# Kernel tuning notes

Hardware: AMD Instinct MI355X
Metric: run time of the kernel (lower is better)

## Reference

```python
import jax, jax.numpy as jnp
import numpy as np

B, C, D, H, W_, CT = 2, 64, 12, 20, 40, 32


def setup_inputs() -> dict:
    key = jax.random.key(0)
    ks = jax.random.split(key, 8)
    def w(k, o, i):
        return jax.random.normal(k, (o, i), jnp.float32) / np.float32(np.sqrt(i))
    return dict(
        x=jax.random.normal(ks[0], (B, C, D, H, W_), jnp.float32),
        preds=jax.random.normal(ks[1], (B, D, H, W_), jnp.float32),
        Wq1=w(ks[2], CT, C), Wq2=w(ks[3], CT, CT),
        Wk1=w(ks[4], CT, C), Wk2=w(ks[5], CT, CT),
        Wv=w(ks[6], CT, C), Wo=w(ks[7], C, CT),
    )


def conv_bn_relu(x, Wm, eps=1e-5):
    # 1x1x1 Conv3d (no bias) + BatchNorm3d (batch stats, no affine) + ReLU
    y = jnp.einsum('bcdhw,oc->bodhw', x, Wm)
    mu = y.mean(axis=(0, 2, 3, 4), keepdims=True)
    var = y.var(axis=(0, 2, 3, 4), keepdims=True)
    return jax.nn.relu((y - mu) * jax.lax.rsqrt(var + eps))


def semantic_gather(x, preds):
    # Vectorized equivalent of the nested batch/disp-class loops:
    # per-pixel argmax over disparity planes, softmax within each argmax group,
    # scatter weighted feature into a dense (b, hw, d, c) tensor (zeros elsewhere).
    b, c, d, h, w = x.shape
    p = jax.nn.softmax(preds, axis=1).reshape(b, d, h * w).transpose(0, 2, 1)  # (b,hw,d)
    f = x.reshape(b, c, d, h * w).transpose(0, 3, 2, 1)                        # (b,hw,d,c)
    a = jnp.argmax(p, axis=-1)                                                 # (b,hw) segment ids
    pv = jnp.take_along_axis(p, a[..., None], axis=-1)[..., 0]                 # (b,hw) gathered prob

    def seg_softmax(vals, segs):
        # softmax over pixels sharing the same argmax disparity class
        m = jax.lax.stop_gradient(jax.ops.segment_max(vals, segs, num_segments=d))
        e = jnp.exp(vals - m[segs])
        s = jax.ops.segment_sum(e, segs, num_segments=d)
        return e / s[segs]

    wt = jax.vmap(seg_softmax)(pv, a)                                          # (b,hw)
    fg = jnp.take_along_axis(f, a[:, :, None, None], axis=2)[:, :, 0, :]       # (b,hw,c)
    oh = jax.nn.one_hot(a, d, dtype=x.dtype)                                   # (b,hw,d)
    feats_sl = oh[..., None] * (fg * wt[..., None])[:, :, None, :]             # (b,hw,d,c)
    return feats_sl.reshape(b, h, w, d, c).transpose(0, 4, 3, 1, 2)            # (b,c,d,h,w)


def reference(x, preds, Wq1, Wq2, Wk1, Wk2, Wv, Wo):
    feats_sl = semantic_gather(x, preds)
    key_feats = feats_sl + x
    # SelfAttentionBlock: query/key = 2 conv-bn-relu, value/out = 1 conv-bn-relu
    q = conv_bn_relu(conv_bn_relu(x, Wq1), Wq2)
    k = conv_bn_relu(conv_bn_relu(key_feats, Wk1), Wk2)
    v = conv_bn_relu(key_feats, Wv)
    b, ct, d, h, w = q.shape
    n = d * h * w
    qf = q.reshape(b, ct, n).transpose(0, 2, 1)   # (b,n,ct)
    kf = k.reshape(b, ct, n)                      # (b,ct,n)
    vf = v.reshape(b, ct, n).transpose(0, 2, 1)   # (b,n,ct)
    sim = jnp.einsum('bnc,bcm->bnm', qf, kf) * (ct ** -0.5)
    sim = jax.nn.softmax(sim, axis=-1)
    ctx = jnp.einsum('bnm,bmc->bnc', sim, vf).transpose(0, 2, 1).reshape(b, ct, d, h, w)
    return conv_bn_relu(ctx, Wo)
```

## Files before the change

### kernel.cpp

```cpp
#include <hip/hip_runtime.h>

#define NB 2
#define CIN 64
#define DD 12
#define HWP 800
#define NPOS 9600
#define CT 32
#define QKSCALE 0.25506601f
#define CSH 11.541560327f

typedef __attribute__((ext_vector_type(8))) short short8;
typedef __attribute__((ext_vector_type(16))) float f32x16;

__device__ __forceinline__ ushort f2bf(float x){
    union { float f; unsigned u; } v; v.f = x;
    unsigned r = v.u + 0x7fffu + ((v.u >> 16) & 1u);
    return (ushort)(r >> 16);
}

__global__ __launch_bounds__(256) void seg_kernel(const float* __restrict__ preds,
                                                  int* __restrict__ a, float* __restrict__ wt)
{
    int b = blockIdx.x / DD, seg = blockIdx.x % DD;
    __shared__ float lpv[HWP];
    __shared__ int   la[HWP];
    __shared__ float red[256];
    int t = threadIdx.x;
    for (int i=t; i<HWP; i+=256){
        const float* p = preds + (size_t)b*DD*HWP + i;
        float mx = -INFINITY; int am = 0;
        #pragma unroll
        for (int d=0; d<DD; ++d){ float v = p[d*HWP]; if (v > mx){ mx=v; am=d; } }
        float s = 0.f;
        #pragma unroll
        for (int d=0; d<DD; ++d) s += __expf(p[d*HWP]-mx);
        lpv[i] = 1.f/s; la[i] = am;
        if (seg == 0) a[b*HWP+i] = am;
    }
    __syncthreads();
    float mx = -INFINITY;
    for (int i=t; i<HWP; i+=256) if (la[i]==seg) mx = fmaxf(mx, lpv[i]);
    red[t]=mx; __syncthreads();
    for (int s=128; s>0; s>>=1){ if (t<s) red[t]=fmaxf(red[t],red[t+s]); __syncthreads(); }
    float m = red[0]; __syncthreads();
    if (m == -INFINITY) return;
    float sm = 0.f;
    for (int i=t; i<HWP; i+=256) if (la[i]==seg) sm += __expf(lpv[i]-m);
    red[t]=sm; __syncthreads();
    for (int s=128; s>0; s>>=1){ if (t<s) red[t]+=red[t+s]; __syncthreads(); }
    float ssum = red[0];
    for (int i=t; i<HWP; i+=256) if (la[i]==seg) wt[b*HWP+i] = __expf(lpv[i]-m)/ssum;
}

__global__ __launch_bounds__(256) void conv1_kernel(const float* __restrict__ x,
    const int* __restrict__ a, const float* __restrict__ wt,
    const float* __restrict__ Wq1, const float* __restrict__ Wk1, const float* __restrict__ Wv,
    float* __restrict__ q1, float* __restrict__ k1, float* __restrict__ v1,
    float* __restrict__ part)
{
    __shared__ float lw[6144];
    for (int i=threadIdx.x; i<2048; i+=256){ lw[i]=Wq1[i]; lw[2048+i]=Wk1[i]; lw[4096+i]=Wv[i]; }
    __syncthreads();
    int t = threadIdx.x;
    int posIdx = blockIdx.x*32 + (t&31);
    int g = t>>5;
    int b = posIdx / NPOS, pos = posIdx % NPOS;
    int d = pos / HWP, pix = pos % HWP;
    float fac = 1.f;
    if (a[b*HWP+pix] == d) fac += wt[b*HWP+pix];
    float acc[12];
    #pragma unroll
    for (int j=0;j<12;++j) acc[j]=0.f;
    const float* xb = x + (size_t)b*CIN*NPOS + pos;
    int chBase = g*12;
    for (int c=0;c<CIN;++c){
        float xv = xb[(size_t)c*NPOS];
        const float* wrow = &lw[chBase*64 + c];
        #pragma unroll
        for (int j=0;j<12;++j) acc[j] += xv * wrow[j*64];
    }
    #pragma unroll
    for (int j=0;j<12;++j){
        int ch = chBase + j;
        float val = acc[j];
        if (ch >= 32) val *= fac;
        acc[j] = val;
        if (ch < 32)       q1[((size_t)b*CT + ch)*NPOS + pos] = val;
        else if (ch < 64)  k1[((size_t)b*CT + (ch-32))*NPOS + pos] = val;
        else               v1[((size_t)b*CT + (ch-64))*NPOS + pos] = val;
    }
    #pragma unroll
    for (int j=0;j<12;++j){
        float s = acc[j], qs = acc[j]*acc[j];
        #pragma unroll
        for (int off=16; off; off>>=1){ s += __shfl_xor(s,off); qs += __shfl_xor(qs,off); }
        if ((t&31)==0){
            int ch = chBase+j;
            part[((size_t)ch*600 + blockIdx.x)*2]   = s;
            part[((size_t)ch*600 + blockIdx.x)*2+1] = qs;
        }
    }
}

__global__ __launch_bounds__(64) void statsfin_kernel(const float* __restrict__ part,
    float* __restrict__ mu, float* __restrict__ rs, int nblk)
{
    int ch = blockIdx.x;
    float s=0.f, q=0.f;
    for (int i=threadIdx.x; i<nblk; i+=64){
        s += part[((size_t)ch*nblk+i)*2];
        q += part[((size_t)ch*nblk+i)*2+1];
    }
    #pragma unroll
    for (int off=32; off; off>>=1){ s += __shfl_xor(s,off); q += __shfl_xor(q,off); }
    if (threadIdx.x==0){
        float m = s/19200.f;
        mu[ch]=m; rs[ch]=rsqrtf(q/19200.f - m*m + 1e-5f);
    }
}

__global__ __launch_bounds__(256) void conv2_kernel(const float* __restrict__ q1, const float* __restrict__ k1,
    const float* __restrict__ Wq2, const float* __restrict__ Wk2,
    const float* __restrict__ mu1, const float* __restrict__ rs1,
    float* __restrict__ q2, float* __restrict__ k2, float* __restrict__ part)
{
    __shared__ float lw[2048];
    for (int i=threadIdx.x; i<1024; i+=256){ lw[i]=Wq2[i]; lw[1024+i]=Wk2[i]; }
    __syncthreads();
    int t = threadIdx.x;
    int posIdx = blockIdx.x*32 + (t&31);
    int g = t>>5;
    int b = posIdx / NPOS, pos = posIdx % NPOS;
    const float* src = (g<4) ? q1 : k1;
    const float* wb  = (g<4) ? lw : (lw+1024);
    float* dst       = (g<4) ? q2 : k2;
    int so = (g<4) ? 0 : 32;
    int chBase = (g&3)*8;
    float acc[8];
    #pragma unroll
    for (int j=0;j<8;++j) acc[j]=0.f;
    for (int c=0;c<32;++c){
        float v = src[((size_t)b*CT + c)*NPOS + pos];
        float vn = fmaxf((v - mu1[so+c])*rs1[so+c], 0.f);
        const float* wrow = &wb[chBase*32 + c];
        #pragma unroll
        for (int j=0;j<8;++j) acc[j] += vn * wrow[j*32];
    }
    #pragma unroll
    for (int j=0;j<8;++j)
        dst[((size_t)b*CT + chBase + j)*NPOS + pos] = acc[j];
    #pragma unroll
    for (int j=0;j<8;++j){
        float s = acc[j], qs = acc[j]*acc[j];
        #pragma unroll
        for (int off=16; off; off>>=1){ s += __shfl_xor(s,off); qs += __shfl_xor(qs,off); }
        if ((t&31)==0){
            int ch = so + chBase + j;
            part[((size_t)ch*600 + blockIdx.x)*2]   = s;
            part[((size_t)ch*600 + blockIdx.x)*2+1] = qs;
        }
    }
}

__global__ __launch_bounds__(256) void pack_kernel(const float* __restrict__ q2, const float* __restrict__ k2,
    const float* __restrict__ v1,
    const float* __restrict__ mu2, const float* __restrict__ rs2,
    const float* __restrict__ muv, const float* __restrict__ rsv,
    ushort* __restrict__ Qbf, ushort* __restrict__ KP, ushort* __restrict__ VP)
{
    if (blockIdx.x < 75){
        int idx = blockIdx.x*256 + threadIdx.x;
        int b = idx / NPOS, pos = idx - b*NPOS;
        const float* qsrc = q2 + (size_t)b*CT*NPOS + pos;
        const float* ksrc = k2 + (size_t)b*CT*NPOS + pos;
        unsigned qw[16], kw[16];
        #pragma unroll
        for (int c2=0; c2<16; ++c2){
            int c0 = 2*c2, c1 = 2*c2+1;
            float a0 = fmaxf((qsrc[(size_t)c0*NPOS] - mu2[c0])*rs2[c0], 0.f)*QKSCALE;
            float a1 = fmaxf((qsrc[(size_t)c1*NPOS] - mu2[c1])*rs2[c1], 0.f)*QKSCALE;
            qw[c2] = (unsigned)f2bf(a0) | ((unsigned)f2bf(a1)<<16);
            float b0 = fmaxf((ksrc[(size_t)c0*NPOS] - mu2[32+c0])*rs2[32+c0], 0.f);
            float b1 = fmaxf((ksrc[(size_t)c1*NPOS] - mu2[32+c1])*rs2[32+c1], 0.f);
            kw[c2] = (unsigned)f2bf(b0) | ((unsigned)f2bf(b1)<<16);
        }
        uint4* qd = (uint4*)(Qbf + (size_t)idx*CT);
        #pragma unroll
        for (int j=0;j<4;++j)
            qd[j] = make_uint4(qw[4*j], qw[4*j+1], qw[4*j+2], qw[4*j+3]);
        int kb = pos >> 5, c = pos & 31;
        ushort* base = KP + ((size_t)(b*300 + kb))*1024;
        *(uint4*)(base + (c)*8)          = make_uint4(kw[0],kw[1],kw[2],kw[3]);
        *(uint4*)(base + (c+32)*8)       = make_uint4(kw[4],kw[5],kw[6],kw[7]);
        *(uint4*)(base + 512 + (c)*8)    = make_uint4(kw[8],kw[9],kw[10],kw[11]);
        *(uint4*)(base + 512 + (c+32)*8) = make_uint4(kw[12],kw[13],kw[14],kw[15]);
    } else {
        int idx = (blockIdx.x-75)*256 + threadIdx.x;
        int b = idx / 38400;
        int r = idx - b*38400;
        int c = r / 1200;
        int g8 = r - c*1200;
        int key = g8*8;
        int kb = g8 >> 2, q8 = g8 & 3;
        int p = q8 >> 1, hh = q8 & 1;
        const float* vs = v1 + ((size_t)b*CT + c)*NPOS + key;
        float m = muv[c], rr = rsv[c];
        unsigned wds[4];
        #pragma unroll
        for (int j=0;j<4;++j){
            float a0 = fmaxf((vs[2*j]   - m)*rr, 0.f);
            float a1 = fmaxf((vs[2*j+1] - m)*rr, 0.f);
            wds[j] = (unsigned)f2bf(a0) | ((unsigned)f2bf(a1)<<16);
        }
        *(uint4*)(VP + ((size_t)(b*300 + kb))*1024 + p*512 + (c + 32*hh)*8)
            = make_uint4(wds[0],wds[1],wds[2],wds[3]);
    }
}

__global__ __launch_bounds__(256) void attn_kernel(const ushort* __restrict__ Qbf,
    const ushort* __restrict__ KP, const ushort* __restrict__ VP,
    float* __restrict__ pacc, float* __restrict__ plsum)
{
    __shared__ float mrg[3][64][17];
    int xcd = blockIdx.x & 7, idx = blockIdx.x >> 3;
    int b = xcd >> 2;
    int qb = (xcd & 3)*75 + idx%75;
    int third = idx/75;
    int q0 = qb*32;
    int t = threadIdx.x, wv = t>>6, l = t&63;
    int c = l & 31, h = l >> 5;

    const char* QbU = (const char*)(Qbf + (size_t)b*NPOS*CT);
    const char* KPb = (const char*)KP;
    const char* VPb = (const char*)VP;

    union U { uint4 u; short8 s; };
    U qf0, qf1;
    qf0.u = *(const uint4*)(QbU + (((q0 + c)*CT + 8*h)<<1));
    qf1.u = *(const uint4*)(QbU + (((q0 + c)*CT + 16 + 8*h)<<1));

    U ones; ones.u = make_uint4(0x3F803F80u,0x3F803F80u,0x3F803F80u,0x3F803F80u);

    f32x16 acc, accl, cinit;
    #pragma unroll
    for (int r=0;r<16;++r){ acc[r]=0.f; accl[r]=0.f; cinit[r]=-CSH; }

    unsigned voff = (unsigned)(l*16);
    unsigned ko = (unsigned)(b*300 + third*100 + wv*25)*2048u;

    U nk0,nk1,nv0,nv1;
    nk0.u = *(const uint4*)(KPb + ko + voff);
    nk1.u = *(const uint4*)(KPb + ko + voff + 1024);
    nv0.u = *(const uint4*)(VPb + ko + voff);
    nv1.u = *(const uint4*)(VPb + ko + voff + 1024);

    for (int ck=0; ck<25; ++ck){
        U ka0=nk0, ka1=nk1, va0=nv0, va1=nv1;
        ko += (ck<24) ? 2048u : 0u;
        nk0.u = *(const uint4*)(KPb + ko + voff);
        nk1.u = *(const uint4*)(KPb + ko + voff + 1024);
        nv0.u = *(const uint4*)(VPb + ko + voff);
        nv1.u = *(const uint4*)(VPb + ko + voff + 1024);

        f32x16 s = __builtin_amdgcn_mfma_f32_32x32x16_bf16(ka0.s, qf0.s, cinit,0,0,0);
        s = __builtin_amdgcn_mfma_f32_32x32x16_bf16(ka1.s, qf1.s, s, 0,0,0);
        float p[16];
        #pragma unroll
        for (int r=0;r<16;++r) asm("v_exp_f32 %0, %1" : "=v"(p[r]) : "v"(s[r]));
        unsigned E0,E1,E2,E3,E4,E5,E6,E7;
        asm("v_cvt_pk_bf16_f32 %0,%1,%2" : "=v"(E0) : "v"(p[0]),  "v"(p[1]));
        asm("v_cvt_pk_bf16_f32 %0,%1,%2" : "=v"(E1) : "v"(p[2]),  "v"(p[3]));
        asm("v_cvt_pk_bf16_f32 %0,%1,%2" : "=v"(E2) : "v"(p[4]),  "v"(p[5]));
        asm("v_cvt_pk_bf16_f32 %0,%1,%2" : "=v"(E3) : "v"(p[6]),  "v"(p[7]));
        asm("v_cvt_pk_bf16_f32 %0,%1,%2" : "=v"(E4) : "v"(p[8]),  "v"(p[9]));
        asm("v_cvt_pk_bf16_f32 %0,%1,%2" : "=v"(E5) : "v"(p[10]), "v"(p[11]));
        asm("v_cvt_pk_bf16_f32 %0,%1,%2" : "=v"(E6) : "v"(p[12]), "v"(p[13]));
        asm("v_cvt_pk_bf16_f32 %0,%1,%2" : "=v"(E7) : "v"(p[14]), "v"(p[15]));
        asm("v_permlane32_swap_b32 %0, %1" : "+v"(E0), "+v"(E2));
        asm("v_permlane32_swap_b32 %0, %1" : "+v"(E1), "+v"(E3));
        asm("v_permlane32_swap_b32 %0, %1" : "+v"(E4), "+v"(E6));
        asm("v_permlane32_swap_b32 %0, %1" : "+v"(E5), "+v"(E7));
        U pf1, pf2;
        pf1.u = make_uint4(E0,E1,E2,E3);
        pf2.u = make_uint4(E4,E5,E6,E7);
        acc  = __builtin_amdgcn_mfma_f32_32x32x16_bf16(va0.s,  pf1.s, acc, 0,0,0);
        accl = __builtin_amdgcn_mfma_f32_32x32x16_bf16(ones.s, pf1.s, accl,0,0,0);
        acc  = __builtin_amdgcn_mfma_f32_32x32x16_bf16(va1.s,  pf2.s, acc, 0,0,0);
        accl = __builtin_amdgcn_mfma_f32_32x32x16_bf16(ones.s, pf2.s, accl,0,0,0);
    }

    float lsum = accl[0];

    if (wv > 0){
        float* mb = &mrg[wv-1][l][0];
        #pragma unroll
        for (int r=0;r<16;++r) mb[r] = acc[r];
        mb[16] = lsum;
    }
    __syncthreads();
    if (wv == 0){
        #pragma unroll
        for (int w2=0; w2<3; ++w2){
            const float* mb = &mrg[w2][l][0];
            #pragma unroll
            for (int r=0;r<16;++r) acc[r] += mb[r];
            lsum += mb[16];
        }
        float* pa = pacc + (size_t)(b*3 + third)*CT*NPOS;
        int pos = q0 + c;
        #pragma unroll
        for (int r=0;r<16;++r){
            int rw = (r&3) + 8*(r>>2) + 4*h;
            pa[(size_t)rw*NPOS + pos] = acc[r];
        }
        if (h == 0) plsum[(size_t)(b*3+third)*NPOS + pos] = lsum;
    }
}

__global__ __launch_bounds__(256) void convo_kernel(const float* __restrict__ pacc,
    const float* __restrict__ plsum, const float* __restrict__ Wo,
    float* __restrict__ outraw, float* __restrict__ part)
{
    __shared__ float lw[2048];
    for (int i=threadIdx.x; i<2048; i+=256) lw[i]=Wo[i];
    __syncthreads();
    int t = threadIdx.x;
    int posIdx = blockIdx.x*32 + (t&31);
    int g = t>>5;
    int b = posIdx / NPOS, pos = posIdx % NPOS;
    const float* pA = pacc + (size_t)(b*3)*CT*NPOS + pos;
    const float* pB = pacc + (size_t)(b*3+1)*CT*NPOS + pos;
    const float* pC = pacc + (size_t)(b*3+2)*CT*NPOS + pos;
    float inv = 1.f/(plsum[(size_t)(b*3)*NPOS + pos] + plsum[(size_t)(b*3+1)*NPOS + pos]
                   + plsum[(size_t)(b*3+2)*NPOS + pos]);
    int chBase = g*8;
    float acc[8];
    #pragma unroll
    for (int j=0;j<8;++j) acc[j]=0.f;
    for (int c=0;c<32;++c){
        float v = (pA[(size_t)c*NPOS] + pB[(size_t)c*NPOS] + pC[(size_t)c*NPOS]) * inv;
        const float* wrow = &lw[chBase*32 + c];
        #pragma unroll
        for (int j=0;j<8;++j) acc[j] += v * wrow[j*32];
    }
    #pragma unroll
    for (int j=0;j<8;++j)
        outraw[((size_t)b*64 + chBase + j)*NPOS + pos] = acc[j];
    #pragma unroll
    for (int j=0;j<8;++j){
        float s = acc[j], qs = acc[j]*acc[j];
        #pragma unroll
        for (int off=16; off; off>>=1){ s += __shfl_xor(s,off); qs += __shfl_xor(qs,off); }
        if ((t&31)==0){
            int ch = chBase+j;
            part[((size_t)ch*600 + blockIdx.x)*2]   = s;
            part[((size_t)ch*600 + blockIdx.x)*2+1] = qs;
        }
    }
}

__global__ __launch_bounds__(256) void bn_relu_kernel(const float* __restrict__ src,
    const float* __restrict__ mu, const float* __restrict__ rs,
    float* __restrict__ dst, int C, int total)
{
    int idx = blockIdx.x*256 + threadIdx.x;
    if (idx >= total) return;
    int ch = (idx / NPOS) % C;
    dst[idx] = fmaxf((src[idx]-mu[ch])*rs[ch], 0.f);
}

extern "C" void kernel_launch(void* const* d_in, const int* in_sizes, int n_in,
                              void* d_out, int out_size, void* d_ws, size_t ws_size,
                              hipStream_t stream)
{
    const float* x     = (const float*)d_in[0];
    const float* preds = (const float*)d_in[1];
    const float* Wq1   = (const float*)d_in[2];
    const float* Wq2   = (const float*)d_in[3];
    const float* Wk1   = (const float*)d_in[4];
    const float* Wk2   = (const float*)d_in[5];
    const float* Wv    = (const float*)d_in[6];
    const float* Wo    = (const float*)d_in[7];
    float* out = (float*)d_out;

    float* w     = (float*)d_ws;
    int*   a_idx = (int*)d_ws;
    float* wt    = w + 4096;
    float* mu1   = w + 6656;
    float* rs1   = w + 6752;
    float* mu2   = w + 6848;
    float* rs2   = w + 6912;
    float* muo   = w + 6976;
    float* rso   = w + 7040;
    float* q1    = w + 8192;
    float* k1    = w + 622592;
    float* v1    = w + 1236992;
    float* q2    = w + 1851392;
    float* k2    = w + 2465792;
    ushort* Qbf  = (ushort*)(w + 8192);
    ushort* KP   = (ushort*)(w + 315392);
    ushort* VP   = (ushort*)(w + 3080192);
    float* pacc  = w + 622592;
    float* plsum = w + 3387392;
    float* part1 = w + 3444992;
    float* part2 = w + 3560192;
    float* parto = w + 3444992;

    seg_kernel  <<<24,  256,0,stream>>>(preds, a_idx, wt);
    conv1_kernel<<<600, 256,0,stream>>>(x, a_idx, wt, Wq1, Wk1, Wv, q1, k1, v1, part1);
    statsfin_kernel<<<96, 64,0,stream>>>(part1, mu1, rs1, 600);
    conv2_kernel<<<600, 256,0,stream>>>(q1, k1, Wq2, Wk2, mu1, rs1, q2, k2, part2);
    statsfin_kernel<<<64, 64,0,stream>>>(part2, mu2, rs2, 600);
    pack_kernel <<<375, 256,0,stream>>>(q2, k2, v1, mu2, rs2, mu1+64, rs1+64, Qbf, KP, VP);
    attn_kernel <<<1800, 256,0,stream>>>(Qbf, KP, VP, pacc, plsum);
    convo_kernel<<<600, 256,0,stream>>>(pacc, plsum, Wo, out, parto);
    statsfin_kernel<<<64, 64,0,stream>>>(parto, muo, rso, 600);
    bn_relu_kernel<<<4800,256,0,stream>>>(out, muo, rso, out, 64, 1228800);
}
```

Measured before the change: 117.6 us.

## Process two 32-query tiles per attention block to reuse K/V loads

Each attention workgroup now handles 64 query positions (two 32-row MFMA tiles) instead of 32, so every K/V chunk loaded from global memory feeds two sets of score/PV MFMAs. The grid is halved to 900 blocks and the XCD-aware block-to-batch mapping is replaced with a plain linear mapping. The intent is to halve K/V global traffic per query and give more independent MFMA/exp work per iteration for latency hiding. The cost is higher register pressure, a doubled LDS merge buffer, and fewer blocks to fill the GPU, which may lower occupancy and L2 locality.

```diff
diff --git a/kernel.cpp b/kernel.cpp
--- a/kernel.cpp
+++ b/kernel.cpp
@@ -221,12 +221,12 @@
     const ushort* __restrict__ KP, const ushort* __restrict__ VP,
     float* __restrict__ pacc, float* __restrict__ plsum)
 {
-    __shared__ float mrg[3][64][17];
-    int xcd = blockIdx.x & 7, idx = blockIdx.x >> 3;
-    int b = xcd >> 2;
-    int qb = (xcd & 3)*75 + idx%75;
-    int third = idx/75;
-    int q0 = qb*32;
+    __shared__ float mrg[3][64][34];
+    int blk = blockIdx.x;
+    int b = blk / 450;
+    int u = blk - b*450;
+    int qb = u % 150, third = u / 150;
+    int q0 = qb*64;
     int t = threadIdx.x, wv = t>>6, l = t&63;
     int c = l & 31, h = l >> 5;
 
@@ -235,15 +235,17 @@
     const char* VPb = (const char*)VP;
 
     union U { uint4 u; short8 s; };
-    U qf0, qf1;
+    U qf0, qf1, qf2, qf3;
     qf0.u = *(const uint4*)(QbU + (((q0 + c)*CT + 8*h)<<1));
     qf1.u = *(const uint4*)(QbU + (((q0 + c)*CT + 16 + 8*h)<<1));
+    qf2.u = *(const uint4*)(QbU + (((q0 + 32 + c)*CT + 8*h)<<1));
+    qf3.u = *(const uint4*)(QbU + (((q0 + 32 + c)*CT + 16 + 8*h)<<1));
 
     U ones; ones.u = make_uint4(0x3F803F80u,0x3F803F80u,0x3F803F80u,0x3F803F80u);
 
-    f32x16 acc, accl, cinit;
-    #pragma unroll
-    for (int r=0;r<16;++r){ acc[r]=0.f; accl[r]=0.f; cinit[r]=-CSH; }
+    f32x16 acc0, acc1, accl0, accl1, cinit;
+    #pragma unroll
+    for (int r=0;r<16;++r){ acc0[r]=0.f; acc1[r]=0.f; accl0[r]=0.f; accl1[r]=0.f; cinit[r]=-CSH; }
 
     unsigned voff = (unsigned)(l*16);
     unsigned ko = (unsigned)(b*300 + third*100 + wv*25)*2048u;
@@ -262,40 +264,70 @@
         nv0.u = *(const uint4*)(VPb + ko + voff);
         nv1.u = *(const uint4*)(VPb + ko + voff + 1024);
 
-        f32x16 s = __builtin_amdgcn_mfma_f32_32x32x16_bf16(ka0.s, qf0.s, cinit,0,0,0);
-        s = __builtin_amdgcn_mfma_f32_32x32x16_bf16(ka1.s, qf1.s, s, 0,0,0);
-        float p[16];
-        #pragma unroll
-        for (int r=0;r<16;++r) asm("v_exp_f32 %0, %1" : "=v"(p[r]) : "v"(s[r]));
-        unsigned E0,E1,E2,E3,E4,E5,E6,E7;
-        asm("v_cvt_pk_bf16_f32 %0,%1,%2" : "=v"(E0) : "v"(p[0]),  "v"(p[1]));
-        asm("v_cvt_pk_bf16_f32 %0,%1,%2" : "=v"(E1) : "v"(p[2]),  "v"(p[3]));
-        asm("v_cvt_pk_bf16_f32 %0,%1,%2" : "=v"(E2) : "v"(p[4]),  "v"(p[5]));
-        asm("v_cvt_pk_bf16_f32 %0,%1,%2" : "=v"(E3) : "v"(p[6]),  "v"(p[7]));
-        asm("v_cvt_pk_bf16_f32 %0,%1,%2" : "=v"(E4) : "v"(p[8]),  "v"(p[9]));
-        asm("v_cvt_pk_bf16_f32 %0,%1,%2" : "=v"(E5) : "v"(p[10]), "v"(p[11]));
-        asm("v_cvt_pk_bf16_f32 %0,%1,%2" : "=v"(E6) : "v"(p[12]), "v"(p[13]));
-        asm("v_cvt_pk_bf16_f32 %0,%1,%2" : "=v"(E7) : "v"(p[14]), "v"(p[15]));
-        asm("v_permlane32_swap_b32 %0, %1" : "+v"(E0), "+v"(E2));
-        asm("v_permlane32_swap_b32 %0, %1" : "+v"(E1), "+v"(E3));
-        asm("v_permlane32_swap_b32 %0, %1" : "+v"(E4), "+v"(E6));
-        asm("v_permlane32_swap_b32 %0, %1" : "+v"(E5), "+v"(E7));
-        U pf1, pf2;
-        pf1.u = make_uint4(E0,E1,E2,E3);
-        pf2.u = make_uint4(E4,E5,E6,E7);
-        acc  = __builtin_amdgcn_mfma_f32_32x32x16_bf16(va0.s,  pf1.s, acc, 0,0,0);
-        accl = __builtin_amdgcn_mfma_f32_32x32x16_bf16(ones.s, pf1.s, accl,0,0,0);
-        acc  = __builtin_amdgcn_mfma_f32_32x32x16_bf16(va1.s,  pf2.s, acc, 0,0,0);
-        accl = __builtin_amdgcn_mfma_f32_32x32x16_bf16(ones.s, pf2.s, accl,0,0,0);
-    }
-
-    float lsum = accl[0];
+        {
+            f32x16 s = __builtin_amdgcn_mfma_f32_32x32x16_bf16(ka0.s, qf0.s, cinit,0,0,0);
+            s = __builtin_amdgcn_mfma_f32_32x32x16_bf16(ka1.s, qf1.s, s, 0,0,0);
+            float p[16];
+            #pragma unroll
+            for (int r=0;r<16;++r) asm("v_exp_f32 %0, %1" : "=v"(p[r]) : "v"(s[r]));
+            unsigned E0,E1,E2,E3,E4,E5,E6,E7;
+            asm("v_cvt_pk_bf16_f32 %0,%1,%2" : "=v"(E0) : "v"(p[0]),  "v"(p[1]));
+            asm("v_cvt_pk_bf16_f32 %0,%1,%2" : "=v"(E1) : "v"(p[2]),  "v"(p[3]));
+            asm("v_cvt_pk_bf16_f32 %0,%1,%2" : "=v"(E2) : "v"(p[4]),  "v"(p[5]));
+            asm("v_cvt_pk_bf16_f32 %0,%1,%2" : "=v"(E3) : "v"(p[6]),  "v"(p[7]));
+            asm("v_cvt_pk_bf16_f32 %0,%1,%2" : "=v"(E4) : "v"(p[8]),  "v"(p[9]));
+            asm("v_cvt_pk_bf16_f32 %0,%1,%2" : "=v"(E5) : "v"(p[10]), "v"(p[11]));
+            asm("v_cvt_pk_bf16_f32 %0,%1,%2" : "=v"(E6) : "v"(p[12]), "v"(p[13]));
+            asm("v_cvt_pk_bf16_f32 %0,%1,%2" : "=v"(E7) : "v"(p[14]), "v"(p[15]));
+            asm("v_permlane32_swap_b32 %0, %1" : "+v"(E0), "+v"(E2));
+            asm("v_permlane32_swap_b32 %0, %1" : "+v"(E1), "+v"(E3));
+            asm("v_permlane32_swap_b32 %0, %1" : "+v"(E4), "+v"(E6));
+            asm("v_permlane32_swap_b32 %0, %1" : "+v"(E5), "+v"(E7));
+            U pf1, pf2;
+            pf1.u = make_uint4(E0,E1,E2,E3);
+            pf2.u = make_uint4(E4,E5,E6,E7);
+            acc0  = __builtin_amdgcn_mfma_f32_32x32x16_bf16(va0.s,  pf1.s, acc0, 0,0,0);
+            accl0 = __builtin_amdgcn_mfma_f32_32x32x16_bf16(ones.s, pf1.s, accl0,0,0,0);
+            acc0  = __builtin_amdgcn_mfma_f32_32x32x16_bf16(va1.s,  pf2.s, acc0, 0,0,0);
+            accl0 = __builtin_amdgcn_mfma_f32_32x32x16_bf16(ones.s, pf2.s, accl0,0,0,0);
+        }
+        {
+            f32x16 s = __builtin_amdgcn_mfma_f32_32x32x16_bf16(ka0.s, qf2.s, cinit,0,0,0);
+            s = __builtin_amdgcn_mfma_f32_32x32x16_bf16(ka1.s, qf3.s, s, 0,0,0);
+            float p[16];
+            #pragma unroll
+            for (int r=0;r<16;++r) asm("v_exp_f32 %0, %1" : "=v"(p[r]) : "v"(s[r]));
+            unsigned E0,E1,E2,E3,E4,E5,E6,E7;
+            asm("v_cvt_pk_bf16_f32 %0,%1,%2" : "=v"(E0) : "v"(p[0]),  "v"(p[1]));
+            asm("v_cvt_pk_bf16_f32 %0,%1,%2" : "=v"(E1) : "v"(p[2]),  "v"(p[3]));
+            asm("v_cvt_pk_bf16_f32 %0,%1,%2" : "=v"(E2) : "v"(p[4]),  "v"(p[5]));
+            asm("v_cvt_pk_bf16_f32 %0,%1,%2" : "=v"(E3) : "v"(p[6]),  "v"(p[7]));
+            asm("v_cvt_pk_bf16_f32 %0,%1,%2" : "=v"(E4) : "v"(p[8]),  "v"(p[9]));
+            asm("v_cvt_pk_bf16_f32 %0,%1,%2" : "=v"(E5) : "v"(p[10]), "v"(p[11]));
+            asm("v_cvt_pk_bf16_f32 %0,%1,%2" : "=v"(E6) : "v"(p[12]), "v"(p[13]));
+            asm("v_cvt_pk_bf16_f32 %0,%1,%2" : "=v"(E7) : "v"(p[14]), "v"(p[15]));
+            asm("v_permlane32_swap_b32 %0, %1" : "+v"(E0), "+v"(E2));
+            asm("v_permlane32_swap_b32 %0, %1" : "+v"(E1), "+v"(E3));
+            asm("v_permlane32_swap_b32 %0, %1" : "+v"(E4), "+v"(E6));
+            asm("v_permlane32_swap_b32 %0, %1" : "+v"(E5), "+v"(E7));
+            U pf1, pf2;
+            pf1.u = make_uint4(E0,E1,E2,E3);
+            pf2.u = make_uint4(E4,E5,E6,E7);
+            acc1  = __builtin_amdgcn_mfma_f32_32x32x16_bf16(va0.s,  pf1.s, acc1, 0,0,0);
+            accl1 = __builtin_amdgcn_mfma_f32_32x32x16_bf16(ones.s, pf1.s, accl1,0,0,0);
+            acc1  = __builtin_amdgcn_mfma_f32_32x32x16_bf16(va1.s,  pf2.s, acc1, 0,0,0);
+            accl1 = __builtin_amdgcn_mfma_f32_32x32x16_bf16(ones.s, pf2.s, accl1,0,0,0);
+        }
+    }
+
+    float lsum0 = accl0[0];
+    float lsum1 = accl1[0];
 
     if (wv > 0){
         float* mb = &mrg[wv-1][l][0];
         #pragma unroll
-        for (int r=0;r<16;++r) mb[r] = acc[r];
-        mb[16] = lsum;
+        for (int r=0;r<16;++r){ mb[r] = acc0[r]; mb[16+r] = acc1[r]; }
+        mb[32] = lsum0; mb[33] = lsum1;
     }
     __syncthreads();
     if (wv == 0){
@@ -303,17 +335,21 @@
         for (int w2=0; w2<3; ++w2){
             const float* mb = &mrg[w2][l][0];
             #pragma unroll
-            for (int r=0;r<16;++r) acc[r] += mb[r];
-            lsum += mb[16];
+            for (int r=0;r<16;++r){ acc0[r] += mb[r]; acc1[r] += mb[16+r]; }
+            lsum0 += mb[32]; lsum1 += mb[33];
         }
         float* pa = pacc + (size_t)(b*3 + third)*CT*NPOS;
-        int pos = q0 + c;
+        int pos0 = q0 + c, pos1 = q0 + 32 + c;
         #pragma unroll
         for (int r=0;r<16;++r){
             int rw = (r&3) + 8*(r>>2) + 4*h;
-            pa[(size_t)rw*NPOS + pos] = acc[r];
-        }
-        if (h == 0) plsum[(size_t)(b*3+third)*NPOS + pos] = lsum;
+            pa[(size_t)rw*NPOS + pos0] = acc0[r];
+            pa[(size_t)rw*NPOS + pos1] = acc1[r];
+        }
+        if (h == 0){
+            plsum[(size_t)(b*3+third)*NPOS + pos0] = lsum0;
+            plsum[(size_t)(b*3+third)*NPOS + pos1] = lsum1;
+        }
     }
 }
 
@@ -412,7 +448,7 @@
     conv2_kernel<<<600, 256,0,stream>>>(q1, k1, Wq2, Wk2, mu1, rs1, q2, k2, part2);
     statsfin_kernel<<<64, 64,0,stream>>>(part2, mu2, rs2, 600);
     pack_kernel <<<375, 256,0,stream>>>(q2, k2, v1, mu2, rs2, mu1+64, rs1+64, Qbf, KP, VP);
-    attn_kernel <<<1800, 256,0,stream>>>(Qbf, KP, VP, pacc, plsum);
+    attn_kernel <<<900, 256,0,stream>>>(Qbf, KP, VP, pacc, plsum);
     convo_kernel<<<600, 256,0,stream>>>(pacc, plsum, Wo, out, parto);
     statsfin_kernel<<<64, 64,0,stream>>>(parto, muo, rso, 600);
     bn_relu_kernel<<<4800,256,0,stream>>>(out, muo, rso, out, 64, 1228800);
```

After: 112.5 us. 1.04x faster.
